# Kernel optimization log

Hardware: AMD Instinct MI355X
Metric: run time of the kernel (lower is better)

Reference implementation:

```python
import jax, jax.numpy as jnp
import numpy as np

R = 2            # connect_gap -> disk radius for morphological closing
N_ITER = 24      # fixed thinning iteration count (jit-compatible stand-in for run-to-convergence)

_yy, _xx = np.mgrid[-R:R + 1, -R:R + 1]
DISK = ((_xx ** 2 + _yy ** 2) <= R * R).astype(np.float32)  # skimage.morphology.disk(2): 5x5, 13 ones
DISK_SUM = float(DISK.sum())


def _conv2d(x, k):
    # x: [D,H,W] float32, k: [kh,kw]; per-slice SAME conv (D acts as batch)
    return jax.lax.conv_general_dilated(x[:, None], k[None, None], (1, 1), 'SAME')[:, 0]


def _closing(mask):
    # binary closing = erosion(dilation(mask)) with disk footprint (zero padding at borders)
    k = jnp.asarray(DISK)
    dil = _conv2d(mask.astype(jnp.float32), k) > 0.5
    ero = _conv2d(dil.astype(jnp.float32), k) > (DISK_SUM - 0.5)
    return ero


def _neighbors(img):
    # 8-neighborhood P2..P9 (N, NE, E, SE, S, SW, W, NW), zero-padded borders
    p = jnp.pad(img, ((0, 0), (1, 1), (1, 1)))
    return (p[:, :-2, 1:-1], p[:, :-2, 2:], p[:, 1:-1, 2:], p[:, 2:, 2:],
            p[:, 2:, 1:-1], p[:, 2:, :-2], p[:, 1:-1, :-2], p[:, :-2, :-2])


def _subiter(img, step):
    # one Zhang-Suen thinning sub-iteration over all slices/voxels at once
    P = _neighbors(img)
    Pi = [q.astype(jnp.int32) for q in P]
    B = sum(Pi)                                   # number of ON neighbors
    seq = Pi + [Pi[0]]
    A = sum(((seq[k] == 0) & (seq[k + 1] == 1)).astype(jnp.int32) for k in range(8))
    cB = (B >= 2) & (B <= 6)
    cA = A == 1
    if step == 0:
        c3 = ~(P[0] & P[2] & P[4])   # P2*P4*P6 == 0
        c4 = ~(P[2] & P[4] & P[6])   # P4*P6*P8 == 0
    else:
        c3 = ~(P[0] & P[2] & P[6])   # P2*P4*P8 == 0
        c4 = ~(P[0] & P[4] & P[6])   # P2*P6*P8 == 0
    return img & ~(img & cB & cA & c3 & c4)


def _skeletonize(mask):
    def body(img, _):
        img = _subiter(img, 0)
        img = _subiter(img, 1)
        return img, None
    out, _ = jax.lax.scan(body, mask, None, length=N_ITER)
    return out


def setup_inputs() -> dict:
    key = jax.random.key(0)
    gt_skel = jax.random.uniform(key, (1, 64, 512, 512), dtype=jnp.float32)
    return {"gt_skel": gt_skel}


def reference(gt_skel):
    mask = gt_skel[0] > 0.5          # squeeze leading dim; binary foreground mask [D,H,W]
    skel = _skeletonize(_closing(mask))
    return skel[None]                # [1,D,H,W] bool
```

## Files before the change

### kernel.cpp

```cpp
#include <hip/hip_runtime.h>
#include <stdint.h>

#define DD    64
#define HH    512
#define WWID  512
#define WPR   8
#define NSUB  48
#define BANDS 4
#define BH    128
#define HALO  52
#define MAXR  (BH + 2*HALO)
#define ARR   (MAXR + 4)
#define PITCH 10

typedef unsigned long long u64;

__global__ void pack_kernel(const float* __restrict__ in, u64* __restrict__ bits) {
    long gid  = (long)blockIdx.x * blockDim.x + threadIdx.x;
    long wv   = gid >> 6;
    int  lane = (int)(gid & 63);
    long base = wv * 256;
    #pragma unroll
    for (int k = 0; k < 4; ++k) {
        float v = in[base + (long)k * 64 + lane];
        u64 m = __ballot(v > 0.5f);
        if (lane == 0) bits[wv * 4 + k] = m;
    }
}

__device__ __forceinline__ u64 zs_word(u64 c, u64 N, u64 NE, u64 E, u64 SE,
                                       u64 S, u64 SW, u64 Wn, u64 NW, int sub) {
    u64 t0 = ~N  & NE;
    u64 t1 = ~NE & E;
    u64 t2 = ~E  & SE;
    u64 t3 = ~SE & S;
    u64 t4 = ~S  & SW;
    u64 t5 = ~SW & Wn;
    u64 t6 = ~Wn & NW;
    u64 t7 = ~NW & N;
    u64 o01 = t0 ^ t1, w01 = t0 & t1;
    u64 o23 = t2 ^ t3, w23 = t2 & t3;
    u64 o45 = t4 ^ t5, w45 = t4 & t5;
    u64 o67 = t6 ^ t7, w67 = t6 & t7;
    u64 oA = o01 ^ o23, wA = w01 | w23 | (o01 & o23);
    u64 oB = o45 ^ o67, wB = w45 | w67 | (o45 & o67);
    u64 A1 = (oA ^ oB) & ~(wA | wB | (oA & oB));
    u64 sa, ca; { u64 tt = N ^ NE; sa = tt ^ E;  ca = (N & NE) | (tt & E);  }
    u64 sb, cb; { u64 tt = SE ^ S; sb = tt ^ SW; cb = (SE & S) | (tt & SW); }
    u64 sc = Wn ^ NW, cc = Wn & NW;
    u64 S0, cd; { u64 tt = sa ^ sb; S0 = tt ^ sc;  cd = (sa & sb) | (tt & sc); }
    u64 t2s, ce; { u64 tt = ca ^ cb; t2s = tt ^ cc; ce = (ca & cb) | (tt & cc); }
    u64 S1 = cd ^ t2s, cf = cd & t2s;
    u64 S2 = ce ^ cf,  S3 = ce & cf;
    u64 cB = (S1 | S2 | S3) & ~((S2 & S1 & S0) | S3);
    u64 c3, c4;
    if (sub == 0) { c3 = ~(N & E & S);  c4 = ~(E & S & Wn); }
    else          { c3 = ~(N & E & Wn); c4 = ~(N & S & Wn); }
    return c & ~(cB & A1 & c3 & c4);
}

#define CLOSE_PHASE(SRC, DST, ISDIL, SETREG) do {                                       \
    if (lr < nrows) {                                                                   \
        u64 w_[5][6];                                                                   \
        _Pragma("unroll") for (int rr = 0; rr < 5; ++rr) {                              \
            ulonglong2 va = *reinterpret_cast<const ulonglong2*>(&SRC[ar-2+rr][h4]);    \
            ulonglong2 vb = *reinterpret_cast<const ulonglong2*>(&SRC[ar-2+rr][h4+2]);  \
            ulonglong2 vc = *reinterpret_cast<const ulonglong2*>(&SRC[ar-2+rr][h4+4]);  \
            w_[rr][0]=va.x; w_[rr][1]=va.y; w_[rr][2]=vb.x;                             \
            w_[rr][3]=vb.y; w_[rr][4]=vc.x; w_[rr][5]=vc.y;                             \
        }                                                                               \
        _Pragma("unroll") for (int jj = 0; jj < 4; ++jj) {                              \
            u64 c=w_[2][jj+1], pl=w_[2][jj], pr=w_[2][jj+2];                            \
            u64 l1=(c<<1)|(pl>>63), l2=(c<<2)|(pl>>62);                                 \
            u64 q1=(c>>1)|(pr<<63), q2=(c>>2)|(pr<<62);                                 \
            u64 u_=w_[1][jj+1], ul=(u_<<1)|(w_[1][jj]>>63), ur=(u_>>1)|(w_[1][jj+2]<<63);\
            u64 d_=w_[3][jj+1], dl=(d_<<1)|(w_[3][jj]>>63), dr=(d_>>1)|(w_[3][jj+2]<<63);\
            u64 u2=w_[0][jj+1], d2=w_[4][jj+1];                                         \
            u64 r_ = ISDIL ? (c|l1|l2|q1|q2|u_|ul|ur|d_|dl|dr|u2|d2)                    \
                           : (c&l1&l2&q1&q2&u_&ul&ur&d_&dl&dr&u2&d2);                   \
            DST[ar][h4+1+jj] = r_;                                                      \
            if (SETREG) { if (jj==0) myw0=r_; else if (jj==1) myw1=r_;                  \
                          else if (jj==2) myw2=r_; else myw3=r_; }                      \
        }                                                                               \
    }                                                                                   \
    __syncthreads();                                                                    \
} while (0)

#define THIN_SUB(SRC, DST, SUB, LO, HI) do {                                            \
    if (lr >= (LO) && lr < (HI)) {                                                      \
        ulonglong2 ua = *reinterpret_cast<const ulonglong2*>(&SRC[ar-1][h4]);           \
        ulonglong2 ub = *reinterpret_cast<const ulonglong2*>(&SRC[ar-1][h4+2]);         \
        ulonglong2 uc = *reinterpret_cast<const ulonglong2*>(&SRC[ar-1][h4+4]);         \
        ulonglong2 da = *reinterpret_cast<const ulonglong2*>(&SRC[ar+1][h4]);           \
        ulonglong2 db = *reinterpret_cast<const ulonglong2*>(&SRC[ar+1][h4+2]);         \
        ulonglong2 dc = *reinterpret_cast<const ulonglong2*>(&SRC[ar+1][h4+4]);         \
        u64 edge = SRC[ar][5 - h];                                                      \
        u64 uu0=ua.x, uu1=ua.y, uu2=ub.x, uu3=ub.y, uu4=uc.x, uu5=uc.y;                 \
        u64 dd0=da.x, dd1=da.y, dd2=db.x, dd3=db.y, dd4=dc.x, dd5=dc.y;                 \
        u64 lw = h ? edge : 0ull;                                                       \
        u64 rw = h ? 0ull : edge;                                                       \
        u64 r0_, r1_, r2_, r3_;                                                         \
        { u64 c=myw0, pl=lw, pr=myw1;                                                   \
          u64 E=(c>>1)|(pr<<63), Wn=(c<<1)|(pl>>63);                                    \
          u64 NE=(uu1>>1)|(uu2<<63), NW=(uu1<<1)|(uu0>>63);                             \
          u64 SE=(dd1>>1)|(dd2<<63), SW=(dd1<<1)|(dd0>>63);                             \
          r0_ = zs_word(c, uu1, NE, E, SE, dd1, SW, Wn, NW, SUB); }                     \
        { u64 c=myw1, pl=myw0, pr=myw2;                                                 \
          u64 E=(c>>1)|(pr<<63), Wn=(c<<1)|(pl>>63);                                    \
          u64 NE=(uu2>>1)|(uu3<<63), NW=(uu2<<1)|(uu1>>63);                             \
          u64 SE=(dd2>>1)|(dd3<<63), SW=(dd2<<1)|(dd1>>63);                             \
          r1_ = zs_word(c, uu2, NE, E, SE, dd2, SW, Wn, NW, SUB); }                     \
        { u64 c=myw2, pl=myw1, pr=myw3;                                                 \
          u64 E=(c>>1)|(pr<<63), Wn=(c<<1)|(pl>>63);                                    \
          u64 NE=(uu3>>1)|(uu4<<63), NW=(uu3<<1)|(uu2>>63);                             \
          u64 SE=(dd3>>1)|(dd4<<63), SW=(dd3<<1)|(dd2>>63);                             \
          r2_ = zs_word(c, uu3, NE, E, SE, dd3, SW, Wn, NW, SUB); }                     \
        { u64 c=myw3, pl=myw2, pr=rw;                                                   \
          u64 E=(c>>1)|(pr<<63), Wn=(c<<1)|(pl>>63);                                    \
          u64 NE=(uu4>>1)|(uu5<<63), NW=(uu4<<1)|(uu3>>63);                             \
          u64 SE=(dd4>>1)|(dd5<<63), SW=(dd4<<1)|(dd3>>63);                             \
          r3_ = zs_word(c, uu4, NE, E, SE, dd4, SW, Wn, NW, SUB); }                     \
        DST[ar][h4+1]=r0_; DST[ar][h4+2]=r1_; DST[ar][h4+3]=r2_; DST[ar][h4+4]=r3_;     \
        myw0=r0_; myw1=r1_; myw2=r2_; myw3=r3_;                                         \
    }                                                                                   \
    __syncthreads();                                                                    \
} while (0)

__global__ __launch_bounds__(512, 1)
void thin_kernel(const u64* __restrict__ bits, int* __restrict__ out) {
    __shared__ u64 bufA[ARR][PITCH];
    __shared__ u64 bufB[ARR][PITCH];

    const int blk  = blockIdx.x;
    const int z    = blk >> 2;
    const int band = blk & 3;
    const int r0   = band * BH;
    const int la   = (r0 - HALO > 0) ? (r0 - HALO) : 0;
    const int lb   = (r0 + BH + HALO < HH) ? (r0 + BH + HALO) : HH;
    const int nrows = lb - la;
    const int ob0  = r0 - la;

    const int t  = threadIdx.x;
    const int lr = t >> 1;
    const int h  = t & 1;
    const int h4 = h * 4;
    const int ar = lr + 2;

    u64 myw0 = 0, myw1 = 0, myw2 = 0, myw3 = 0;

    {
        u64* fa = &bufA[0][0];
        u64* fb = &bufB[0][0];
        for (int i = t; i < ARR * PITCH; i += 512) { fa[i] = 0; fb[i] = 0; }
    }
    __syncthreads();

    if (lr < nrows) {
        const u64* src = bits + ((long)(z * HH + la + lr)) * WPR + h4;
        ulonglong2 v0 = *reinterpret_cast<const ulonglong2*>(src);
        ulonglong2 v1 = *reinterpret_cast<const ulonglong2*>(src + 2);
        bufA[ar][h4 + 1] = v0.x;
        bufA[ar][h4 + 2] = v0.y;
        bufA[ar][h4 + 3] = v1.x;
        bufA[ar][h4 + 4] = v1.y;
    }
    __syncthreads();

    CLOSE_PHASE(bufA, bufB, 1, 0);
    CLOSE_PHASE(bufB, bufA, 0, 1);

    #pragma unroll 1
    for (int it2 = 0; it2 < NSUB / 2; ++it2) {
        {
            int hw = NSUB - (2 * it2 + 1);
            int lo = ob0 - hw;       if (lo < 0) lo = 0;
            int hi = ob0 + BH + hw;  if (hi > nrows) hi = nrows;
            THIN_SUB(bufA, bufB, 0, lo, hi);
        }
        {
            int hw = NSUB - (2 * it2 + 2);
            int lo = ob0 - hw;       if (lo < 0) lo = 0;
            int hi = ob0 + BH + hw;  if (hi > nrows) hi = nrows;
            THIN_SUB(bufB, bufA, 1, lo, hi);
        }
    }

    const long slice_base = (long)z * HH * WWID;
    for (int e = t; e < BH * (WWID / 4); e += 512) {
        int rr  = e >> 7;
        int x4  = e & 127;
        int gr  = r0 + rr;
        int arr = (gr - la) + 2;
        int col = x4 * 4;
        u64 w  = bufA[arr][1 + (col >> 6)];
        int sh = col & 63;
        int4 f;
        f.x = (int)((w >> (sh + 0)) & 1ull);
        f.y = (int)((w >> (sh + 1)) & 1ull);
        f.z = (int)((w >> (sh + 2)) & 1ull);
        f.w = (int)((w >> (sh + 3)) & 1ull);
        *reinterpret_cast<int4*>(out + slice_base + (long)gr * WWID + col) = f;
    }
}

extern "C" void kernel_launch(void* const* d_in, const int* in_sizes, int n_in,
                              void* d_out, int out_size, void* d_ws, size_t ws_size,
                              hipStream_t stream) {
    const float* in   = (const float*)d_in[0];
    int*         out  = (int*)d_out;
    u64*         bits = (u64*)d_ws;

    pack_kernel<<<16384, 256, 0, stream>>>(in, bits);
    thin_kernel<<<DD * BANDS, 512, 0, stream>>>(bits, out);
}
```

Baseline: 127.3 us.

## Replace per-subiteration block barriers with neighbor-wave counter synchronization

Thinning rows are remapped so each wavefront owns a contiguous strip of 29 rows. The block-wide __syncthreads after every Zhang-Suen sub-iteration is replaced by point-to-point waits: a wave spins on LDS counters published by its two adjacent waves, then releases its own counter when its step is done. The aim is to cut full-block barrier stalls and let waves drift relative to each other. In exchange it adds spin-polling with s_sleep, leaves a few lanes idle per wave, and depends on acquire/release ordering in LDS being enough for correctness.

```diff
diff --git a/kernel.cpp b/kernel.cpp
--- a/kernel.cpp
+++ b/kernel.cpp
@@ -12,6 +12,7 @@
 #define MAXR  (BH + 2*HALO)
 #define ARR   (MAXR + 4)
 #define PITCH 10
+#define RPW   29
 
 typedef unsigned long long u64;
 
@@ -60,7 +61,7 @@
 }
 
 #define CLOSE_PHASE(SRC, DST, ISDIL, SETREG) do {                                       \
-    if (lr < nrows) {                                                                   \
+    if (act) {                                                                          \
         u64 w_[5][6];                                                                   \
         _Pragma("unroll") for (int rr = 0; rr < 5; ++rr) {                              \
             ulonglong2 va = *reinterpret_cast<const ulonglong2*>(&SRC[ar-2+rr][h4]);    \
@@ -86,50 +87,66 @@
     __syncthreads();                                                                    \
 } while (0)
 
-#define THIN_SUB(SRC, DST, SUB, LO, HI) do {                                            \
-    if (lr >= (LO) && lr < (HI)) {                                                      \
-        ulonglong2 ua = *reinterpret_cast<const ulonglong2*>(&SRC[ar-1][h4]);           \
-        ulonglong2 ub = *reinterpret_cast<const ulonglong2*>(&SRC[ar-1][h4+2]);         \
-        ulonglong2 uc = *reinterpret_cast<const ulonglong2*>(&SRC[ar-1][h4+4]);         \
-        ulonglong2 da = *reinterpret_cast<const ulonglong2*>(&SRC[ar+1][h4]);           \
-        ulonglong2 db = *reinterpret_cast<const ulonglong2*>(&SRC[ar+1][h4+2]);         \
-        ulonglong2 dc = *reinterpret_cast<const ulonglong2*>(&SRC[ar+1][h4+4]);         \
-        u64 edge = SRC[ar][5 - h];                                                      \
-        u64 uu0=ua.x, uu1=ua.y, uu2=ub.x, uu3=ub.y, uu4=uc.x, uu5=uc.y;                 \
-        u64 dd0=da.x, dd1=da.y, dd2=db.x, dd3=db.y, dd4=dc.x, dd5=dc.y;                 \
-        u64 lw = h ? edge : 0ull;                                                       \
-        u64 rw = h ? 0ull : edge;                                                       \
-        u64 r0_, r1_, r2_, r3_;                                                         \
-        { u64 c=myw0, pl=lw, pr=myw1;                                                   \
-          u64 E=(c>>1)|(pr<<63), Wn=(c<<1)|(pl>>63);                                    \
-          u64 NE=(uu1>>1)|(uu2<<63), NW=(uu1<<1)|(uu0>>63);                             \
-          u64 SE=(dd1>>1)|(dd2<<63), SW=(dd1<<1)|(dd0>>63);                             \
-          r0_ = zs_word(c, uu1, NE, E, SE, dd1, SW, Wn, NW, SUB); }                     \
-        { u64 c=myw1, pl=myw0, pr=myw2;                                                 \
-          u64 E=(c>>1)|(pr<<63), Wn=(c<<1)|(pl>>63);                                    \
-          u64 NE=(uu2>>1)|(uu3<<63), NW=(uu2<<1)|(uu1>>63);                             \
-          u64 SE=(dd2>>1)|(dd3<<63), SW=(dd2<<1)|(dd1>>63);                             \
-          r1_ = zs_word(c, uu2, NE, E, SE, dd2, SW, Wn, NW, SUB); }                     \
-        { u64 c=myw2, pl=myw1, pr=myw3;                                                 \
-          u64 E=(c>>1)|(pr<<63), Wn=(c<<1)|(pl>>63);                                    \
-          u64 NE=(uu3>>1)|(uu4<<63), NW=(uu3<<1)|(uu2>>63);                             \
-          u64 SE=(dd3>>1)|(dd4<<63), SW=(dd3<<1)|(dd2>>63);                             \
-          r2_ = zs_word(c, uu3, NE, E, SE, dd3, SW, Wn, NW, SUB); }                     \
-        { u64 c=myw3, pl=myw2, pr=rw;                                                   \
-          u64 E=(c>>1)|(pr<<63), Wn=(c<<1)|(pl>>63);                                    \
-          u64 NE=(uu4>>1)|(uu5<<63), NW=(uu4<<1)|(uu3>>63);                             \
-          u64 SE=(dd4>>1)|(dd5<<63), SW=(dd4<<1)|(dd3>>63);                             \
-          r3_ = zs_word(c, uu4, NE, E, SE, dd4, SW, Wn, NW, SUB); }                     \
-        DST[ar][h4+1]=r0_; DST[ar][h4+2]=r1_; DST[ar][h4+3]=r2_; DST[ar][h4+4]=r3_;     \
-        myw0=r0_; myw1=r1_; myw2=r2_; myw3=r3_;                                         \
+#define THIN_STEP(SRC, DST, SUB, K) do {                                                \
+    {   const int need = (K) - 1;                                                       \
+        for (;;) {                                                                      \
+            int a_ = (w > 0) ? __hip_atomic_load(&cnt[w-1], __ATOMIC_ACQUIRE,           \
+                                 __HIP_MEMORY_SCOPE_WORKGROUP) : need;                  \
+            int b_ = (w < 7) ? __hip_atomic_load(&cnt[w+1], __ATOMIC_ACQUIRE,           \
+                                 __HIP_MEMORY_SCOPE_WORKGROUP) : need;                  \
+            if (a_ >= need && b_ >= need) break;                                        \
+            __builtin_amdgcn_s_sleep(1);                                                \
+        }                                                                               \
     }                                                                                   \
-    __syncthreads();                                                                    \
+    {   const int hw = NSUB - (K);                                                      \
+        int lo = ob0 - hw;       if (lo < 0) lo = 0;                                    \
+        int hi = ob0 + BH + hw;  if (hi > nrows) hi = nrows;                            \
+        if (act && lr >= lo && lr < hi) {                                               \
+            ulonglong2 ua = *reinterpret_cast<const ulonglong2*>(&SRC[ar-1][h4]);       \
+            ulonglong2 ub = *reinterpret_cast<const ulonglong2*>(&SRC[ar-1][h4+2]);     \
+            ulonglong2 uc = *reinterpret_cast<const ulonglong2*>(&SRC[ar-1][h4+4]);     \
+            ulonglong2 da = *reinterpret_cast<const ulonglong2*>(&SRC[ar+1][h4]);       \
+            ulonglong2 db = *reinterpret_cast<const ulonglong2*>(&SRC[ar+1][h4+2]);     \
+            ulonglong2 dc = *reinterpret_cast<const ulonglong2*>(&SRC[ar+1][h4+4]);     \
+            u64 edge = SRC[ar][5 - h];                                                  \
+            u64 uu0=ua.x, uu1=ua.y, uu2=ub.x, uu3=ub.y, uu4=uc.x, uu5=uc.y;             \
+            u64 dd0=da.x, dd1=da.y, dd2=db.x, dd3=db.y, dd4=dc.x, dd5=dc.y;             \
+            u64 lw = h ? edge : 0ull;                                                   \
+            u64 rw = h ? 0ull : edge;                                                   \
+            u64 r0_, r1_, r2_, r3_;                                                     \
+            { u64 c=myw0, pl=lw, pr=myw1;                                               \
+              u64 E=(c>>1)|(pr<<63), Wn=(c<<1)|(pl>>63);                                \
+              u64 NE=(uu1>>1)|(uu2<<63), NW=(uu1<<1)|(uu0>>63);                         \
+              u64 SE=(dd1>>1)|(dd2<<63), SW=(dd1<<1)|(dd0>>63);                         \
+              r0_ = zs_word(c, uu1, NE, E, SE, dd1, SW, Wn, NW, SUB); }                 \
+            { u64 c=myw1, pl=myw0, pr=myw2;                                             \
+              u64 E=(c>>1)|(pr<<63), Wn=(c<<1)|(pl>>63);                                \
+              u64 NE=(uu2>>1)|(uu3<<63), NW=(uu2<<1)|(uu1>>63);                         \
+              u64 SE=(dd2>>1)|(dd3<<63), SW=(dd2<<1)|(dd1>>63);                         \
+              r1_ = zs_word(c, uu2, NE, E, SE, dd2, SW, Wn, NW, SUB); }                 \
+            { u64 c=myw2, pl=myw1, pr=myw3;                                             \
+              u64 E=(c>>1)|(pr<<63), Wn=(c<<1)|(pl>>63);                                \
+              u64 NE=(uu3>>1)|(uu4<<63), NW=(uu3<<1)|(uu2>>63);                         \
+              u64 SE=(dd3>>1)|(dd4<<63), SW=(dd3<<1)|(dd2>>63);                         \
+              r2_ = zs_word(c, uu3, NE, E, SE, dd3, SW, Wn, NW, SUB); }                 \
+            { u64 c=myw3, pl=myw2, pr=rw;                                               \
+              u64 E=(c>>1)|(pr<<63), Wn=(c<<1)|(pl>>63);                                \
+              u64 NE=(uu4>>1)|(uu5<<63), NW=(uu4<<1)|(uu3>>63);                         \
+              u64 SE=(dd4>>1)|(dd5<<63), SW=(dd4<<1)|(dd3>>63);                         \
+              r3_ = zs_word(c, uu4, NE, E, SE, dd4, SW, Wn, NW, SUB); }                 \
+            DST[ar][h4+1]=r0_; DST[ar][h4+2]=r1_; DST[ar][h4+3]=r2_; DST[ar][h4+4]=r3_; \
+            myw0=r0_; myw1=r1_; myw2=r2_; myw3=r3_;                                     \
+        }                                                                               \
+    }                                                                                   \
+    if (lane == 0)                                                                      \
+        __hip_atomic_store(&cnt[w], (K), __ATOMIC_RELEASE, __HIP_MEMORY_SCOPE_WORKGROUP);\
 } while (0)
 
 __global__ __launch_bounds__(512, 1)
 void thin_kernel(const u64* __restrict__ bits, int* __restrict__ out) {
     __shared__ u64 bufA[ARR][PITCH];
     __shared__ u64 bufB[ARR][PITCH];
+    __shared__ int cnt[8];
 
     const int blk  = blockIdx.x;
     const int z    = blk >> 2;
@@ -140,11 +157,15 @@
     const int nrows = lb - la;
     const int ob0  = r0 - la;
 
-    const int t  = threadIdx.x;
-    const int lr = t >> 1;
-    const int h  = t & 1;
-    const int h4 = h * 4;
-    const int ar = lr + 2;
+    const int t    = threadIdx.x;
+    const int w    = t >> 6;
+    const int lane = t & 63;
+    const int lrl  = lane >> 1;
+    const int lr   = w * RPW + lrl;
+    const int h    = lane & 1;
+    const int h4   = h * 4;
+    const int ar   = lr + 2;
+    const bool act = (lrl < RPW) && (lr < nrows);
 
     u64 myw0 = 0, myw1 = 0, myw2 = 0, myw3 = 0;
 
@@ -152,10 +173,11 @@
         u64* fa = &bufA[0][0];
         u64* fb = &bufB[0][0];
         for (int i = t; i < ARR * PITCH; i += 512) { fa[i] = 0; fb[i] = 0; }
+        if (t < 8) cnt[t] = 0;
     }
     __syncthreads();
 
-    if (lr < nrows) {
+    if (act) {
         const u64* src = bits + ((long)(z * HH + la + lr)) * WPR + h4;
         ulonglong2 v0 = *reinterpret_cast<const ulonglong2*>(src);
         ulonglong2 v1 = *reinterpret_cast<const ulonglong2*>(src + 2);
@@ -171,19 +193,10 @@
 
     #pragma unroll 1
     for (int it2 = 0; it2 < NSUB / 2; ++it2) {
-        {
-            int hw = NSUB - (2 * it2 + 1);
-            int lo = ob0 - hw;       if (lo < 0) lo = 0;
-            int hi = ob0 + BH + hw;  if (hi > nrows) hi = nrows;
-            THIN_SUB(bufA, bufB, 0, lo, hi);
-        }
-        {
-            int hw = NSUB - (2 * it2 + 2);
-            int lo = ob0 - hw;       if (lo < 0) lo = 0;
-            int hi = ob0 + BH + hw;  if (hi > nrows) hi = nrows;
-            THIN_SUB(bufB, bufA, 1, lo, hi);
-        }
-    }
+        THIN_STEP(bufA, bufB, 0, 2 * it2 + 1);
+        THIN_STEP(bufB, bufA, 1, 2 * it2 + 2);
+    }
+    __syncthreads();
 
     const long slice_base = (long)z * HH * WWID;
     for (int e = t; e < BH * (WWID / 4); e += 512) {
@@ -192,13 +205,13 @@
         int gr  = r0 + rr;
         int arr = (gr - la) + 2;
         int col = x4 * 4;
-        u64 w  = bufA[arr][1 + (col >> 6)];
+        u64 wv  = bufA[arr][1 + (col >> 6)];
         int sh = col & 63;
         int4 f;
-        f.x = (int)((w >> (sh + 0)) & 1ull);
-        f.y = (int)((w >> (sh + 1)) & 1ull);
-        f.z = (int)((w >> (sh + 2)) & 1ull);
-        f.w = (int)((w >> (sh + 3)) & 1ull);
+        f.x = (int)((wv >> (sh + 0)) & 1ull);
+        f.y = (int)((wv >> (sh + 1)) & 1ull);
+        f.z = (int)((wv >> (sh + 2)) & 1ull);
+        f.w = (int)((wv >> (sh + 3)) & 1ull);
         *reinterpret_cast<int4*>(out + slice_base + (long)gr * WWID + col) = f;
     }
 }
```

After: 142.2 us. 1.12x slower.

## Split each row across four threads with 1024-thread blocks in thinning kernel

Applied to the files above, without the earlier changes.

Each image row is now handled by four threads owning two 64-bit words each, instead of two threads owning four words. Blocks grow to 1024 threads. The shared-memory pitch widens to 14 with an offset of 2 so that each thread's neighbor words are read as aligned 16-byte vectors, and edge words come from zero-padded columns instead of a select. The intent is more parallelism per block and more latency hiding over the 48 serialized sub-iterations. In exchange, each thread loads proportionally more halo words and each barrier now spans more waves.

```diff
diff --git a/kernel.cpp b/kernel.cpp
--- a/kernel.cpp
+++ b/kernel.cpp
@@ -11,7 +11,9 @@
 #define HALO  52
 #define MAXR  (BH + 2*HALO)
 #define ARR   (MAXR + 4)
-#define PITCH 10
+#define PITCH 14
+#define WOFF  2
+#define NTHR  1024
 
 typedef unsigned long long u64;
 
@@ -60,73 +62,65 @@
 }
 
 #define CLOSE_PHASE(SRC, DST, ISDIL, SETREG) do {                                       \
-    if (lr < nrows) {                                                                   \
-        u64 w_[5][6];                                                                   \
+    if (act) {                                                                          \
+        u64 s_[5][6];                                                                   \
         _Pragma("unroll") for (int rr = 0; rr < 5; ++rr) {                              \
-            ulonglong2 va = *reinterpret_cast<const ulonglong2*>(&SRC[ar-2+rr][h4]);    \
-            ulonglong2 vb = *reinterpret_cast<const ulonglong2*>(&SRC[ar-2+rr][h4+2]);  \
-            ulonglong2 vc = *reinterpret_cast<const ulonglong2*>(&SRC[ar-2+rr][h4+4]);  \
-            w_[rr][0]=va.x; w_[rr][1]=va.y; w_[rr][2]=vb.x;                             \
-            w_[rr][3]=vb.y; w_[rr][4]=vc.x; w_[rr][5]=vc.y;                             \
+            ulonglong2 v0 = *reinterpret_cast<const ulonglong2*>(&SRC[ar-2+rr][wb-2]);  \
+            ulonglong2 v1 = *reinterpret_cast<const ulonglong2*>(&SRC[ar-2+rr][wb]);    \
+            ulonglong2 v2 = *reinterpret_cast<const ulonglong2*>(&SRC[ar-2+rr][wb+2]);  \
+            s_[rr][0]=v0.x; s_[rr][1]=v0.y; s_[rr][2]=v1.x;                             \
+            s_[rr][3]=v1.y; s_[rr][4]=v2.x; s_[rr][5]=v2.y;                             \
         }                                                                               \
-        _Pragma("unroll") for (int jj = 0; jj < 4; ++jj) {                              \
-            u64 c=w_[2][jj+1], pl=w_[2][jj], pr=w_[2][jj+2];                            \
-            u64 l1=(c<<1)|(pl>>63), l2=(c<<2)|(pl>>62);                                 \
-            u64 q1=(c>>1)|(pr<<63), q2=(c>>2)|(pr<<62);                                 \
-            u64 u_=w_[1][jj+1], ul=(u_<<1)|(w_[1][jj]>>63), ur=(u_>>1)|(w_[1][jj+2]<<63);\
-            u64 d_=w_[3][jj+1], dl=(d_<<1)|(w_[3][jj]>>63), dr=(d_>>1)|(w_[3][jj+2]<<63);\
-            u64 u2=w_[0][jj+1], d2=w_[4][jj+1];                                         \
-            u64 r_ = ISDIL ? (c|l1|l2|q1|q2|u_|ul|ur|d_|dl|dr|u2|d2)                    \
-                           : (c&l1&l2&q1&q2&u_&ul&ur&d_&dl&dr&u2&d2);                   \
-            DST[ar][h4+1+jj] = r_;                                                      \
-            if (SETREG) { if (jj==0) myw0=r_; else if (jj==1) myw1=r_;                  \
-                          else if (jj==2) myw2=r_; else myw3=r_; }                      \
+        u64 rA, rB;                                                                     \
+        _Pragma("unroll") for (int jj = 0; jj < 2; ++jj) {                              \
+            u64 c  = s_[2][jj+2], pl = s_[2][jj+1], pr = s_[2][jj+3];                   \
+            u64 l1 = (c<<1)|(pl>>63), l2 = (c<<2)|(pl>>62);                             \
+            u64 r1 = (c>>1)|(pr<<63), r2 = (c>>2)|(pr<<62);                             \
+            u64 u_ = s_[1][jj+2], ul = (u_<<1)|(s_[1][jj+1]>>63), ur = (u_>>1)|(s_[1][jj+3]<<63);\
+            u64 d_ = s_[3][jj+2], dl = (d_<<1)|(s_[3][jj+1]>>63), dr = (d_>>1)|(s_[3][jj+3]<<63);\
+            u64 u2 = s_[0][jj+2], d2 = s_[4][jj+2];                                     \
+            u64 r_ = ISDIL ? (c|l1|l2|r1|r2|u_|ul|ur|d_|dl|dr|u2|d2)                    \
+                           : (c&l1&l2&r1&r2&u_&ul&ur&d_&dl&dr&u2&d2);                   \
+            if (jj == 0) rA = r_; else rB = r_;                                         \
         }                                                                               \
+        ulonglong2 st; st.x = rA; st.y = rB;                                            \
+        *reinterpret_cast<ulonglong2*>(&DST[ar][wb]) = st;                              \
+        if (SETREG) { myw0 = rA; myw1 = rB; }                                           \
     }                                                                                   \
     __syncthreads();                                                                    \
 } while (0)
 
 #define THIN_SUB(SRC, DST, SUB, LO, HI) do {                                            \
-    if (lr >= (LO) && lr < (HI)) {                                                      \
-        ulonglong2 ua = *reinterpret_cast<const ulonglong2*>(&SRC[ar-1][h4]);           \
-        ulonglong2 ub = *reinterpret_cast<const ulonglong2*>(&SRC[ar-1][h4+2]);         \
-        ulonglong2 uc = *reinterpret_cast<const ulonglong2*>(&SRC[ar-1][h4+4]);         \
-        ulonglong2 da = *reinterpret_cast<const ulonglong2*>(&SRC[ar+1][h4]);           \
-        ulonglong2 db = *reinterpret_cast<const ulonglong2*>(&SRC[ar+1][h4+2]);         \
-        ulonglong2 dc = *reinterpret_cast<const ulonglong2*>(&SRC[ar+1][h4+4]);         \
-        u64 edge = SRC[ar][5 - h];                                                      \
-        u64 uu0=ua.x, uu1=ua.y, uu2=ub.x, uu3=ub.y, uu4=uc.x, uu5=uc.y;                 \
-        u64 dd0=da.x, dd1=da.y, dd2=db.x, dd3=db.y, dd4=dc.x, dd5=dc.y;                 \
-        u64 lw = h ? edge : 0ull;                                                       \
-        u64 rw = h ? 0ull : edge;                                                       \
-        u64 r0_, r1_, r2_, r3_;                                                         \
-        { u64 c=myw0, pl=lw, pr=myw1;                                                   \
-          u64 E=(c>>1)|(pr<<63), Wn=(c<<1)|(pl>>63);                                    \
-          u64 NE=(uu1>>1)|(uu2<<63), NW=(uu1<<1)|(uu0>>63);                             \
-          u64 SE=(dd1>>1)|(dd2<<63), SW=(dd1<<1)|(dd0>>63);                             \
-          r0_ = zs_word(c, uu1, NE, E, SE, dd1, SW, Wn, NW, SUB); }                     \
-        { u64 c=myw1, pl=myw0, pr=myw2;                                                 \
-          u64 E=(c>>1)|(pr<<63), Wn=(c<<1)|(pl>>63);                                    \
-          u64 NE=(uu2>>1)|(uu3<<63), NW=(uu2<<1)|(uu1>>63);                             \
-          u64 SE=(dd2>>1)|(dd3<<63), SW=(dd2<<1)|(dd1>>63);                             \
-          r1_ = zs_word(c, uu2, NE, E, SE, dd2, SW, Wn, NW, SUB); }                     \
-        { u64 c=myw2, pl=myw1, pr=myw3;                                                 \
-          u64 E=(c>>1)|(pr<<63), Wn=(c<<1)|(pl>>63);                                    \
-          u64 NE=(uu3>>1)|(uu4<<63), NW=(uu3<<1)|(uu2>>63);                             \
-          u64 SE=(dd3>>1)|(dd4<<63), SW=(dd3<<1)|(dd2>>63);                             \
-          r2_ = zs_word(c, uu3, NE, E, SE, dd3, SW, Wn, NW, SUB); }                     \
-        { u64 c=myw3, pl=myw2, pr=rw;                                                   \
-          u64 E=(c>>1)|(pr<<63), Wn=(c<<1)|(pl>>63);                                    \
-          u64 NE=(uu4>>1)|(uu5<<63), NW=(uu4<<1)|(uu3>>63);                             \
-          u64 SE=(dd4>>1)|(dd5<<63), SW=(dd4<<1)|(dd3>>63);                             \
-          r3_ = zs_word(c, uu4, NE, E, SE, dd4, SW, Wn, NW, SUB); }                     \
-        DST[ar][h4+1]=r0_; DST[ar][h4+2]=r1_; DST[ar][h4+3]=r2_; DST[ar][h4+4]=r3_;     \
-        myw0=r0_; myw1=r1_; myw2=r2_; myw3=r3_;                                         \
+    if (act && lr >= (LO) && lr < (HI)) {                                               \
+        ulonglong2 u0 = *reinterpret_cast<const ulonglong2*>(&SRC[ar-1][wb-2]);         \
+        ulonglong2 u1 = *reinterpret_cast<const ulonglong2*>(&SRC[ar-1][wb]);           \
+        ulonglong2 u2 = *reinterpret_cast<const ulonglong2*>(&SRC[ar-1][wb+2]);         \
+        ulonglong2 d0 = *reinterpret_cast<const ulonglong2*>(&SRC[ar+1][wb-2]);         \
+        ulonglong2 d1 = *reinterpret_cast<const ulonglong2*>(&SRC[ar+1][wb]);           \
+        ulonglong2 d2 = *reinterpret_cast<const ulonglong2*>(&SRC[ar+1][wb+2]);         \
+        ulonglong2 cl = *reinterpret_cast<const ulonglong2*>(&SRC[ar][wb-2]);           \
+        ulonglong2 cr = *reinterpret_cast<const ulonglong2*>(&SRC[ar][wb+2]);           \
+        u64 rA, rB;                                                                     \
+        { u64 c = myw0, pl = cl.y, pr = myw1;                                           \
+          u64 N  = u1.x, S = d1.x;                                                      \
+          u64 E  = (c>>1)|(pr<<63),   Wn = (c<<1)|(pl>>63);                             \
+          u64 NE = (u1.x>>1)|(u1.y<<63), NW = (u1.x<<1)|(u0.y>>63);                     \
+          u64 SE = (d1.x>>1)|(d1.y<<63), SW = (d1.x<<1)|(d0.y>>63);                     \
+          rA = zs_word(c, N, NE, E, SE, S, SW, Wn, NW, SUB); }                          \
+        { u64 c = myw1, pl = myw0, pr = cr.x;                                           \
+          u64 N  = u1.y, S = d1.y;                                                      \
+          u64 E  = (c>>1)|(pr<<63),   Wn = (c<<1)|(pl>>63);                             \
+          u64 NE = (u1.y>>1)|(u2.x<<63), NW = (u1.y<<1)|(u1.x>>63);                     \
+          u64 SE = (d1.y>>1)|(d2.x<<63), SW = (d1.y<<1)|(d1.x>>63);                     \
+          rB = zs_word(c, N, NE, E, SE, S, SW, Wn, NW, SUB); }                          \
+        ulonglong2 st; st.x = rA; st.y = rB;                                            \
+        *reinterpret_cast<ulonglong2*>(&DST[ar][wb]) = st;                              \
+        myw0 = rA; myw1 = rB;                                                           \
     }                                                                                   \
     __syncthreads();                                                                    \
 } while (0)
 
-__global__ __launch_bounds__(512, 1)
+__global__ __launch_bounds__(NTHR, 1)
 void thin_kernel(const u64* __restrict__ bits, int* __restrict__ out) {
     __shared__ u64 bufA[ARR][PITCH];
     __shared__ u64 bufB[ARR][PITCH];
@@ -141,28 +135,25 @@
     const int ob0  = r0 - la;
 
     const int t  = threadIdx.x;
-    const int lr = t >> 1;
-    const int h  = t & 1;
-    const int h4 = h * 4;
+    const int lr = t >> 2;
+    const int q  = t & 3;
+    const int wb = 2 * q + WOFF;
     const int ar = lr + 2;
-
-    u64 myw0 = 0, myw1 = 0, myw2 = 0, myw3 = 0;
+    const bool act = (lr < nrows);
+
+    u64 myw0 = 0, myw1 = 0;
 
     {
         u64* fa = &bufA[0][0];
         u64* fb = &bufB[0][0];
-        for (int i = t; i < ARR * PITCH; i += 512) { fa[i] = 0; fb[i] = 0; }
+        for (int i = t; i < ARR * PITCH; i += NTHR) { fa[i] = 0; fb[i] = 0; }
     }
     __syncthreads();
 
-    if (lr < nrows) {
-        const u64* src = bits + ((long)(z * HH + la + lr)) * WPR + h4;
-        ulonglong2 v0 = *reinterpret_cast<const ulonglong2*>(src);
-        ulonglong2 v1 = *reinterpret_cast<const ulonglong2*>(src + 2);
-        bufA[ar][h4 + 1] = v0.x;
-        bufA[ar][h4 + 2] = v0.y;
-        bufA[ar][h4 + 3] = v1.x;
-        bufA[ar][h4 + 4] = v1.y;
+    if (act) {
+        const u64* src = bits + ((long)(z * HH + la + lr)) * WPR + 2 * q;
+        ulonglong2 v = *reinterpret_cast<const ulonglong2*>(src);
+        *reinterpret_cast<ulonglong2*>(&bufA[ar][wb]) = v;
     }
     __syncthreads();
 
@@ -186,13 +177,13 @@
     }
 
     const long slice_base = (long)z * HH * WWID;
-    for (int e = t; e < BH * (WWID / 4); e += 512) {
+    for (int e = t; e < BH * (WWID / 4); e += NTHR) {
         int rr  = e >> 7;
         int x4  = e & 127;
         int gr  = r0 + rr;
         int arr = (gr - la) + 2;
         int col = x4 * 4;
-        u64 w  = bufA[arr][1 + (col >> 6)];
+        u64 w  = bufA[arr][WOFF + (col >> 6)];
         int sh = col & 63;
         int4 f;
         f.x = (int)((w >> (sh + 0)) & 1ull);
@@ -211,5 +202,5 @@
     u64*         bits = (u64*)d_ws;
 
     pack_kernel<<<16384, 256, 0, stream>>>(in, bits);
-    thin_kernel<<<DD * BANDS, 512, 0, stream>>>(bits, out);
-}
+    thin_kernel<<<DD * BANDS, NTHR, 0, stream>>>(bits, out);
+}
```

Result: faster. 121.1 us (-4.9%).
